# Kernel optimization log

Hardware: AMD Instinct MI355X
Metric: run time of the kernel (lower is better)

## Reference

```python
import jax, jax.numpy as jnp
import numpy as np

EMBED = 1024
HEADS = 16
HEAD_DIM = EMBED // HEADS
HIDDEN = 4096
EPS = 1e-5


def setup_inputs() -> dict:
    key = jax.random.key(0)
    ks = jax.random.split(key, 16)
    s_e = 1.0 / np.sqrt(EMBED)
    s_h = 1.0 / np.sqrt(HIDDEN)
    return {
        "x": jax.random.normal(ks[0], (8, 1024, EMBED), dtype=jnp.float32),
        "ln1_g": jnp.ones((EMBED,), jnp.float32),
        "ln1_b": jnp.zeros((EMBED,), jnp.float32),
        "ln2_g": jnp.ones((EMBED,), jnp.float32),
        "ln2_b": jnp.zeros((EMBED,), jnp.float32),
        "wq": jax.random.uniform(ks[1], (EMBED, EMBED), jnp.float32, -s_e, s_e),
        "bq": jax.random.uniform(ks[2], (EMBED,), jnp.float32, -s_e, s_e),
        "wk": jax.random.uniform(ks[3], (EMBED, EMBED), jnp.float32, -s_e, s_e),
        "bk": jax.random.uniform(ks[4], (EMBED,), jnp.float32, -s_e, s_e),
        "wv": jax.random.uniform(ks[5], (EMBED, EMBED), jnp.float32, -s_e, s_e),
        "bv": jax.random.uniform(ks[6], (EMBED,), jnp.float32, -s_e, s_e),
        "wo": jax.random.uniform(ks[7], (EMBED, EMBED), jnp.float32, -s_e, s_e),
        "bo": jax.random.uniform(ks[8], (EMBED,), jnp.float32, -s_e, s_e),
        "w1": jax.random.uniform(ks[9], (EMBED, HIDDEN), jnp.float32, -s_e, s_e),
        "b1": jax.random.uniform(ks[10], (HIDDEN,), jnp.float32, -s_e, s_e),
        "w2": jax.random.uniform(ks[11], (HIDDEN, EMBED), jnp.float32, -s_h, s_h),
        "b2": jax.random.uniform(ks[12], (EMBED,), jnp.float32, -s_h, s_h),
    }


def _layernorm(x, g, b):
    mu = jnp.mean(x, axis=-1, keepdims=True)
    var = jnp.mean((x - mu) ** 2, axis=-1, keepdims=True)
    return (x - mu) * jax.lax.rsqrt(var + EPS) * g + b


def reference(x, ln1_g, ln1_b, ln2_g, ln2_b, wq, bq, wk, bk, wv, bv, wo, bo, w1, b1, w2, b2):
    B, N, E = x.shape
    scale = HEAD_DIM ** (-0.5)
    # --- attention sublayer (pre-norm) ---
    h = _layernorm(x, ln1_g, ln1_b)
    q = (h @ wq + bq).reshape(B, N, HEADS, HEAD_DIM).transpose(0, 2, 1, 3) * scale
    k = (h @ wk + bk).reshape(B, N, HEADS, HEAD_DIM).transpose(0, 2, 1, 3)
    v = (h @ wv + bv).reshape(B, N, HEADS, HEAD_DIM).transpose(0, 2, 1, 3)
    scores = jnp.einsum("bhqd,bhkd->bhqk", q, k)
    attn = jax.nn.softmax(scores, axis=-1)
    ctx = jnp.einsum("bhqk,bhkd->bhqd", attn, v)
    ctx = ctx.transpose(0, 2, 1, 3).reshape(B, N, E)
    x = x + (ctx @ wo + bo)
    # --- FFN sublayer (pre-norm) ---
    h2 = _layernorm(x, ln2_g, ln2_b)
    ff = jax.nn.relu(h2 @ w1 + b1) @ w2 + b2
    return x + ff
```

## Files before the change

kernel.cpp:

```cpp
#include <hip/hip_runtime.h>
#include <hip/hip_bf16.h>

typedef __attribute__((ext_vector_type(4))) float f32x4;
typedef __attribute__((ext_vector_type(16))) float f32x16;
typedef __attribute__((ext_vector_type(8))) __bf16 bf16x8;
typedef __attribute__((ext_vector_type(4))) __bf16 bf16x4;
typedef __attribute__((ext_vector_type(4))) unsigned int u32x4;

static constexpr int E    = 1024;
static constexpr int TOK  = 8192;
static constexpr int HID  = 4096;

#define DEVINL __device__ __forceinline__

DEVINL void gload16(const void* g, void* l) {
  __builtin_amdgcn_global_load_lds((__attribute__((address_space(1))) void*)g,
                                   (__attribute__((address_space(3))) void*)l, 16, 0, 0);
}

#define ABAR()  asm volatile("s_barrier" ::: "memory")
#define AVM(n)  asm volatile("s_waitcnt vmcnt(" #n ")" ::: "memory")
#define ALGKM0() asm volatile("s_waitcnt lgkmcnt(0)")
#define CVTPK(dst, lo, hi) asm("v_cvt_pk_bf16_f32 %0, %1, %2" : "=v"(dst) : "v"(lo), "v"(hi))
#define PLSWAP(a, b) asm("v_permlane32_swap_b32 %0, %1" : "+v"(a), "+v"(b))

template <int N> DEVINL void avm() {
  if constexpr (N == 0)      asm volatile("s_waitcnt vmcnt(0)" ::: "memory");
  else if constexpr (N == 2) asm volatile("s_waitcnt vmcnt(2)" ::: "memory");
  else if constexpr (N == 6) asm volatile("s_waitcnt vmcnt(6)" ::: "memory");
  else if constexpr (N == 8) asm volatile("s_waitcnt vmcnt(8)" ::: "memory");
  else if constexpr (N == 9) asm volatile("s_waitcnt vmcnt(9)" ::: "memory");
  else                       asm volatile("s_waitcnt vmcnt(0)" ::: "memory");
}

__global__ __launch_bounds__(256) void wconv6_kernel(const float* __restrict__ wq,
                                                     const float* __restrict__ wk,
                                                     const float* __restrict__ wv,
                                                     const float* __restrict__ wo,
                                                     const float* __restrict__ w1,
                                                     const float* __restrict__ w2,
                                                     __bf16* __restrict__ Wqkv,
                                                     __bf16* __restrict__ Wot,
                                                     __bf16* __restrict__ W1t,
                                                     __bf16* __restrict__ W2t) {
  const int id = blockIdx.x;
  const float* W; __bf16* Wt; int K, N, lid;
  if (id < 1024)      { W = wq; Wt = Wqkv;                K = 1024; N = 1024; lid = id; }
  else if (id < 2048) { W = wk; Wt = Wqkv + 1024 * 1024;  K = 1024; N = 1024; lid = id - 1024; }
  else if (id < 3072) { W = wv; Wt = Wqkv + 2048 * 1024;  K = 1024; N = 1024; lid = id - 2048; }
  else if (id < 4096) { W = wo; Wt = Wot;                 K = 1024; N = 1024; lid = id - 3072; }
  else if (id < 8192) { W = w1; Wt = W1t;                 K = 1024; N = 4096; lid = id - 4096; }
  else                { W = w2; Wt = W2t;                 K = 4096; N = 1024; lid = id - 8192; }
  const int nx = N >> 5;
  const long n0 = (long)(lid % nx) * 32;
  const long k0 = (long)(lid / nx) * 32;

  __shared__ float tile[32][33];
  const int t  = threadIdx.x;
  const int r  = t >> 3;
  const int c4 = (t & 7) * 4;
  float4 v = *(const float4*)&W[(k0 + r) * N + n0 + c4];
  tile[r][c4 + 0] = v.x; tile[r][c4 + 1] = v.y;
  tile[r][c4 + 2] = v.z; tile[r][c4 + 3] = v.w;
  __syncthreads();
  bf16x4 o;
#pragma unroll
  for (int i = 0; i < 4; ++i) o[i] = (__bf16)tile[c4 + i][r];
  *(bf16x4*)&Wt[(n0 + r) * K + k0 + c4] = o;
}

__global__ __launch_bounds__(256) void ln_kernel(const float* __restrict__ X,
                                                 const float* __restrict__ g,
                                                 const float* __restrict__ be,
                                                 __bf16* __restrict__ O) {
  const int t = threadIdx.x;
  const long row = blockIdx.x;
  float4 v = *(const float4*)&X[row * E + t * 4];
  float s  = v.x + v.y + v.z + v.w;
  float ss = v.x * v.x + v.y * v.y + v.z * v.z + v.w * v.w;
#pragma unroll
  for (int off = 32; off; off >>= 1) {
    s  += __shfl_down(s, off);
    ss += __shfl_down(ss, off);
  }
  __shared__ float red[8];
  const int w = t >> 6;
  if ((t & 63) == 0) { red[w] = s; red[4 + w] = ss; }
  __syncthreads();
  s  = red[0] + red[1] + red[2] + red[3];
  ss = red[4] + red[5] + red[6] + red[7];
  const float mean = s * (1.0f / E);
  const float var  = ss * (1.0f / E) - mean * mean;
  const float rstd = rsqrtf(var + 1e-5f);
  float4 gv = *(const float4*)&g[t * 4];
  float4 bv = *(const float4*)&be[t * 4];
  bf16x4 o;
  o[0] = (__bf16)((v.x - mean) * rstd * gv.x + bv.x);
  o[1] = (__bf16)((v.y - mean) * rstd * gv.y + bv.y);
  o[2] = (__bf16)((v.z - mean) * rstd * gv.z + bv.z);
  o[3] = (__bf16)((v.w - mean) * rstd * gv.w + bv.w);
  *(bf16x4*)&O[row * E + t * 4] = o;
}

__global__ __launch_bounds__(256) void reduce2_kernel(float* __restrict__ out,
                                                      const __bf16* __restrict__ t0,
                                                      const __bf16* __restrict__ t1,
                                                      const float* __restrict__ b2) {
  const int i = blockIdx.x * 256 + threadIdx.x;
  float4 o = ((const float4*)out)[i];
  bf16x4 a = ((const bf16x4*)t0)[i];
  bf16x4 b = ((const bf16x4*)t1)[i];
  float4 bb = ((const float4*)b2)[i & 255];
  o.x += bb.x + (float)a[0] + (float)b[0];
  o.y += bb.y + (float)a[1] + (float)b[1];
  o.z += bb.z + (float)a[2] + (float)b[2];
  o.w += bb.w + (float)a[3] + (float)b[3];
  ((float4*)out)[i] = o;
}

template <bool RELU, bool RESID, bool OUTBF, int NB>
__global__ __launch_bounds__(512, 2) void gemm8p_kernel(const __bf16* __restrict__ A,
                                                        const __bf16* __restrict__ Bt,
                                                        const float* __restrict__ bias0,
                                                        const float* __restrict__ bias1,
                                                        const float* __restrict__ bias2,
                                                        const float* resid,
                                                        void* Cout, void* Cout2,
                                                        int M, int N, int K, int KLD) {
  extern __shared__ char lds[];
  const int tid  = threadIdx.x;
  const int lane = tid & 63;
  const int l15  = lane & 15;
  const int kp   = lane >> 4;
  const int wid  = tid >> 6;
  const int wr   = wid >> 2;
  const int wc   = wid & 3;

  const int gx   = gridDim.x, gy = gridDim.y;
  const int nwg  = gx * gy * gridDim.z;
  const int flat = blockIdx.x + gx * (blockIdx.y + gy * blockIdx.z);
  const int swz  = (flat & 7) * (nwg >> 3) + (flat >> 3);
  const int bx   = swz % gx;
  const int by   = (swz / gx) % gy;
  const int bz   = swz / (gx * gy);
  const long brow = (long)by * 256;
  const long bcol = (long)bx * 256;
  const long koff = (long)bz * K;

  const __bf16* Ab = A  + brow * KLD + koff;
  const __bf16* Bb = Bt + bcol * KLD + koff;
  void* Cdst = bz ? Cout2 : Cout;
  const int NT = K >> 6;

  auto stageU = [&](const __bf16* Gb, int rc0, int k0, int dstOff) {
#pragma unroll
    for (int i = 0; i < 2; ++i) {
      const int c = i * 512 + tid;
      const int r = c >> 3;
      const int p = (c & 7) ^ (r & 7);
      gload16(Gb + (long)(rc0 + r) * KLD + k0 + p * 8, lds + dstOff + c * 16);
    }
  };

  f32x4 acc[8][4];
  const f32x4 z4 = {0.f, 0.f, 0.f, 0.f};
#pragma unroll
  for (int m = 0; m < 8; ++m)
#pragma unroll
    for (int n = 0; n < 4; ++n) acc[m][n] = z4;

  bf16x8 af[4][2], bh0[2][2], bh1[2][2];

  auto readA = [&](int off) {
#pragma unroll
    for (int mm = 0; mm < 4; ++mm)
#pragma unroll
      for (int kk = 0; kk < 2; ++kk) {
        const int lr = mm * 32 + wr * 16 + l15;
        const int p  = ((kk << 2) + kp) ^ (lr & 7);
        af[mm][kk] = *(const bf16x8*)(lds + off + lr * 128 + p * 16);
      }
  };
  auto readB = [&](int off, bf16x8 (*bf)[2]) {
#pragma unroll
    for (int nn = 0; nn < 2; ++nn)
#pragma unroll
      for (int kk = 0; kk < 2; ++kk) {
        const int lc = nn * 64 + wc * 16 + l15;
        const int p  = ((kk << 2) + kp) ^ (lc & 7);
        bf[nn][kk] = *(const bf16x8*)(lds + off + lc * 128 + p * 16);
      }
  };
  auto quad = [&](int mb, int nb, bf16x8 (*bf)[2]) {
    __builtin_amdgcn_s_setprio(1);
#pragma unroll
    for (int kk = 0; kk < 2; ++kk)
#pragma unroll
      for (int mm = 0; mm < 4; ++mm)
#pragma unroll
        for (int nn = 0; nn < 2; ++nn)
          acc[mb + mm][nb + nn] = __builtin_amdgcn_mfma_f32_16x16x32_bf16(
              af[mm][kk], bf[nn][kk], acc[mb + mm][nb + nn], 0, 0, 0);
    __builtin_amdgcn_s_setprio(0);
  };

  stageU(Ab, 0,   0, 0);
  stageU(Bb, 0,   0, 32768);
  stageU(Bb, 128, 0, 49152);
  stageU(Ab, 128, 0, 16384);
  stageU(Ab, 0,   64, 65536 + 0);
  stageU(Bb, 0,   64, 65536 + 32768);
  stageU(Bb, 128, 64, 65536 + 49152);
  avm<6>();
  ABAR();

  for (int t = 0; t < NT; ++t) {
    const int cb  = (t & 1) ? 65536 : 0;
    const int nb1 = cb ^ 65536;
    const int k1 = (t + 1 < NT) ? ((t + 1) << 6) : 0;
    const int k2 = (t + 2 < NT) ? ((t + 2) << 6) : 0;

    readA(cb + 0);
    readB(cb + 32768, bh0);
    stageU(Ab, 128, k1, nb1 + 16384);
    ABAR(); ALGKM0();
    quad(0, 0, bh0);
    ABAR();

    readB(cb + 49152, bh1);
    stageU(Ab, 0, k2, cb + 0);
    ABAR(); ALGKM0();
    quad(0, 2, bh1);
    ABAR();

    readA(cb + 16384);
    stageU(Bb, 0, k2, cb + 32768);
    ABAR(); ALGKM0();
    quad(4, 0, bh0);
    ABAR();

    stageU(Bb, 128, k2, cb + 49152);
    avm<6>();
    ABAR();
    quad(4, 2, bh1);
    ABAR();
  }
  avm<0>();

#pragma unroll
  for (int m = 0; m < 8; ++m) {
#pragma unroll
    for (int n = 0; n < 4; ++n) {
      const long col = bcol + n * 64 + wc * 16 + l15;
      float bb;
      if (NB == 3) {
        const float* bp = (col < 1024) ? bias0 : ((col < 2048) ? bias1 : bias2);
        bb = bp[col & 1023];
      } else if (NB == 1) {
        bb = bias0[col];
      } else {
        bb = 0.f;
      }
#pragma unroll
      for (int j = 0; j < 4; ++j) {
        const long row = brow + m * 32 + wr * 16 + (lane >> 4) * 4 + j;
        float val = acc[m][n][j] + bb;
        if (RELU) val = fmaxf(val, 0.f);
        const long idx = row * N + col;
        if (RESID) val += resid[idx];
        if (OUTBF) ((__bf16*)Cdst)[idx] = (__bf16)val;
        else       ((float*)Cdst)[idx]  = val;
      }
    }
  }
}

template <int BM_, int DEPTH, bool RELU, bool RESID, bool OUTBF, int NB>
__global__ __launch_bounds__(512, 2) void gemmk_kernel(const __bf16* __restrict__ A,
                                                       const __bf16* __restrict__ Bt,
                                                       const float* __restrict__ bias0,
                                                       const float* __restrict__ bias1,
                                                       const float* __restrict__ bias2,
                                                       const float* resid,
                                                       void* Cout, void* Cout2,
                                                       int M, int N, int K, int KLD) {
  extern __shared__ char lds[];
  constexpr int MF    = BM_ / 32;
  constexpr int ABYT  = BM_ * 64;
  constexpr int TILEB = ABYT + 16384;
  constexpr int AL    = BM_ / 128;
  constexpr int TL    = AL + 2;
  constexpr int W     = (DEPTH - 2) * TL;

  const int tid  = threadIdx.x;
  const int lane = tid & 63;
  const int l15  = lane & 15;
  const int kp   = lane >> 4;
  const int wid  = tid >> 6;
  const int wr   = wid >> 2;
  const int wc   = wid & 3;

  const int gx   = gridDim.x, gy = gridDim.y;
  const int nwg  = gx * gy * gridDim.z;
  const int flat = blockIdx.x + gx * (blockIdx.y + gy * blockIdx.z);
  const int swz  = (flat & 7) * (nwg >> 3) + (flat >> 3);
  const int bx   = swz % gx;
  const int by   = (swz / gx) % gy;
  const int bz   = swz / (gx * gy);
  const long brow = (long)by * BM_;
  const long bcol = (long)bx * 256;
  const long koff = (long)bz * K;

  const __bf16* Ab = A  + brow * KLD + koff;
  const __bf16* Bb = Bt + bcol * KLD + koff;
  void* Cdst = bz ? Cout2 : Cout;
  const int NT = K >> 5;

  auto stageA = [&](int k0, char* dst) {
#pragma unroll
    for (int i = 0; i < AL; ++i) {
      const int c = i * 512 + tid;
      const int r = c >> 2;
      const int p = (c & 3) ^ ((r >> 1) & 3);
      gload16(Ab + (long)r * KLD + k0 + p * 8, dst + c * 16);
    }
  };
  auto stageB = [&](int k0, char* dst) {
#pragma unroll
    for (int i = 0; i < 2; ++i) {
      const int c = i * 512 + tid;
      const int r = c >> 2;
      const int p = (c & 3) ^ ((r >> 1) & 3);
      gload16(Bb + (long)r * KLD + k0 + p * 8, dst + c * 16);
    }
  };

  f32x4 acc[MF][4];
  const f32x4 z4 = {0.f, 0.f, 0.f, 0.f};
#pragma unroll
  for (int m = 0; m < MF; ++m)
#pragma unroll
    for (int n = 0; n < 4; ++n) acc[m][n] = z4;

#pragma unroll
  for (int pt = 0; pt < DEPTH - 1; ++pt) {
    stageA(pt * 32, lds + pt * TILEB);
    stageB(pt * 32, lds + pt * TILEB + ABYT);
  }

  bf16x8 af[4], bfr[4];

  for (int t = 0; t < NT; ++t) {
    const int cb = t % DEPTH;
    const int sb = (t + DEPTH - 1) % DEPTH;
    const char* Ac = lds + cb * TILEB;
    const char* Bc = Ac + ABYT;
    char* An = lds + sb * TILEB;
    const int kt = (t + DEPTH - 1 < NT) ? ((t + DEPTH - 1) << 5) : 0;

    avm<W>();
    ABAR();

#pragma unroll
    for (int m = 0; m < 4; ++m) {
      const int row = m * 32 + wr * 16 + l15;
      af[m] = *(const bf16x8*)(Ac + row * 64 + (kp ^ ((row >> 1) & 3)) * 16);
    }
#pragma unroll
    for (int n = 0; n < 4; ++n) {
      const int col = n * 64 + wc * 16 + l15;
      bfr[n] = *(const bf16x8*)(Bc + col * 64 + (kp ^ ((col >> 1) & 3)) * 16);
    }
    stageA(kt, An);
    stageB(kt, An + ABYT);
    ABAR(); ALGKM0();
    __builtin_amdgcn_s_setprio(1);
#pragma unroll
    for (int m = 0; m < 4; ++m)
#pragma unroll
      for (int n = 0; n < 4; ++n)
        acc[m][n] = __builtin_amdgcn_mfma_f32_16x16x32_bf16(af[m], bfr[n], acc[m][n], 0, 0, 0);
    __builtin_amdgcn_s_setprio(0);
  }
  avm<0>();

#pragma unroll
  for (int m = 0; m < MF; ++m) {
#pragma unroll
    for (int n = 0; n < 4; ++n) {
      const long col = bcol + n * 64 + wc * 16 + l15;
      float bb;
      if (NB == 3) {
        const float* bp = (col < 1024) ? bias0 : ((col < 2048) ? bias1 : bias2);
        bb = bp[col & 1023];
      } else if (NB == 1) {
        bb = bias0[col];
      } else {
        bb = 0.f;
      }
#pragma unroll
      for (int j = 0; j < 4; ++j) {
        const long row = brow + m * 32 + wr * 16 + (lane >> 4) * 4 + j;
        float val = acc[m][n][j] + bb;
        if (RELU) val = fmaxf(val, 0.f);
        const long idx = row * N + col;
        if (RESID) val += resid[idx];
        if (OUTBF) ((__bf16*)Cdst)[idx] = (__bf16)val;
        else       ((float*)Cdst)[idx]  = val;
      }
    }
  }
}

__global__ __launch_bounds__(256, 3) void attn_kernel(const __bf16* __restrict__ QKV,
                                                      __bf16* __restrict__ Og) {
  __shared__ __align__(16) __bf16 Qs[128 * 64];
  __shared__ __align__(16) __bf16 Ks[2][64 * 64];
  __shared__ __align__(16) __bf16 Vt[2][64 * 64];

  const int QSTR = 3072;
  const int t    = threadIdx.x;
  const int lane = t & 63;
  const int w    = t >> 6;
  const int l31  = lane & 31;
  const int h    = lane >> 5;
  const int b    = blockIdx.y >> 4;
  const int hh   = blockIdx.y & 15;
  const long row0 = (long)b * 1024 + (long)blockIdx.x * 128;
  const long kvrow0 = (long)b * 1024;
  const int colQ = hh * 64;
  const int colK = colQ + 1024;
  const int colV = colQ + 2048;

#pragma unroll
  for (int j = 0; j < 4; ++j) {
    const int c = j * 256 + t;
    const int r = c >> 3;
    const int p = (c & 7) ^ (r & 7);
    gload16(QKV + (row0 + r) * QSTR + colQ + p * 8, (char*)Qs + c * 16);
  }
#pragma unroll
  for (int j = 0; j < 2; ++j) {
    const int c = j * 256 + t;
    const int r = c >> 3;
    const int p = (c & 7) ^ (r & 7);
    gload16(QKV + (kvrow0 + r) * QSTR + colK + p * 8, (char*)Ks[0] + c * 16);
  }
  bf16x8 vv[2];
#pragma unroll
  for (int j = 0; j < 2; ++j) {
    const int c = j * 256 + t;
    const int key = c >> 3, dc = c & 7;
    vv[j] = *(const bf16x8*)(QKV + (kvrow0 + key) * QSTR + colV + dc * 8);
  }
  AVM(0);
#pragma unroll
  for (int j = 0; j < 2; ++j) {
    const int c = j * 256 + t;
    const int key = c >> 3, dc = c & 7;
#pragma unroll
    for (int e = 0; e < 8; ++e) {
      const int d = dc * 8 + e;
      *(__bf16*)((char*)Vt[0] + d * 128 + (((key >> 3) ^ dc) * 16) + (key & 7) * 2) = vv[j][e];
    }
  }
  __syncthreads();

  bf16x8 bq[4];
  {
    const int qrow = w * 32 + l31;
#pragma unroll
    for (int kk = 0; kk < 4; ++kk) {
      const int p = (kk * 2 + h) ^ (qrow & 7);
      bq[kk] = *(const bf16x8*)((const char*)Qs + qrow * 128 + p * 16);
    }
  }

  f32x16 ctx0, ctx1;
#pragma unroll
  for (int r = 0; r < 16; ++r) { ctx0[r] = 0.f; ctx1[r] = 0.f; }
  float m = -INFINITY, l = 0.f;

  for (int kb = 0; kb < 16; ++kb) {
    const int cur = kb & 1, nxt = cur ^ 1;
    const int kb1 = (kb + 1 < 16) ? kb + 1 : kb;
    const long kr1 = kvrow0 + kb1 * 64;

#pragma unroll
    for (int j = 0; j < 2; ++j) {
      const int c = j * 256 + t;
      const int key = c >> 3, dc = c & 7;
      vv[j] = *(const bf16x8*)(QKV + (kr1 + key) * QSTR + colV + dc * 8);
    }
#pragma unroll
    for (int j = 0; j < 2; ++j) {
      const int c = j * 256 + t;
      const int r = c >> 3;
      const int p = (c & 7) ^ (r & 7);
      gload16(QKV + (kr1 + r) * QSTR + colK + p * 8, (char*)Ks[nxt] + c * 16);
    }

    f32x16 s0, s1;
#pragma unroll
    for (int r = 0; r < 16; ++r) { s0[r] = 0.f; s1[r] = 0.f; }
    __builtin_amdgcn_s_setprio(1);
#pragma unroll
    for (int kk = 0; kk < 4; ++kk) {
      const int pce = kk * 2 + h;
      const int p0i = pce ^ (l31 & 7);
      bf16x8 ak0 = *(const bf16x8*)((const char*)Ks[cur] + l31 * 128 + p0i * 16);
      bf16x8 ak1 = *(const bf16x8*)((const char*)Ks[cur] + (32 + l31) * 128 + p0i * 16);
      s0 = __builtin_amdgcn_mfma_f32_32x32x16_bf16(ak0, bq[kk], s0, 0, 0, 0);
      s1 = __builtin_amdgcn_mfma_f32_32x32x16_bf16(ak1, bq[kk], s1, 0, 0, 0);
    }
    __builtin_amdgcn_s_setprio(0);

    float mx = s0[0];
#pragma unroll
    for (int r = 1; r < 16; ++r) mx = fmaxf(mx, s0[r]);
#pragma unroll
    for (int r = 0; r < 16; ++r) mx = fmaxf(mx, s1[r]);
    mx = fmaxf(mx, __shfl_xor(mx, 32));

    if (!__all(mx - m <= 64.f)) {
      const float mn = fmaxf(m, mx);
      const float corr = __expf((m - mn) * 0.125f);
      l *= corr;
#pragma unroll
      for (int r = 0; r < 16; ++r) { ctx0[r] *= corr; ctx1[r] *= corr; }
      m = mn;
    }
    f32x16 p0, p1;
    float rs = 0.f;
#pragma unroll
    for (int r = 0; r < 16; ++r) { p0[r] = __expf((s0[r] - m) * 0.125f); rs += p0[r]; }
#pragma unroll
    for (int r = 0; r < 16; ++r) { p1[r] = __expf((s1[r] - m) * 0.125f); rs += p1[r]; }
    rs += __shfl_xor(rs, 32);
    l += rs;

    AVM(2);
#pragma unroll
    for (int j = 0; j < 2; ++j) {
      const int c = j * 256 + t;
      const int key = c >> 3, dc = c & 7;
#pragma unroll
      for (int e = 0; e < 8; ++e) {
        const int d = dc * 8 + e;
        *(__bf16*)((char*)Vt[nxt] + d * 128 + (((key >> 3) ^ dc) * 16) + (key & 7) * 2) = vv[j][e];
      }
    }

    bf16x8 paf[4];
#pragma unroll
    for (int ks = 0; ks < 4; ++ks) {
      const int base = (ks & 1) * 8;
      unsigned a0, a1, b0, b1;
      if (ks < 2) {
        CVTPK(a0, p0[base + 0], p0[base + 1]);
        CVTPK(b0, p0[base + 4], p0[base + 5]);
        CVTPK(a1, p0[base + 2], p0[base + 3]);
        CVTPK(b1, p0[base + 6], p0[base + 7]);
      } else {
        CVTPK(a0, p1[base + 0], p1[base + 1]);
        CVTPK(b0, p1[base + 4], p1[base + 5]);
        CVTPK(a1, p1[base + 2], p1[base + 3]);
        CVTPK(b1, p1[base + 6], p1[base + 7]);
      }
      PLSWAP(a0, b0);
      PLSWAP(a1, b1);
      u32x4 wv4; wv4[0] = a0; wv4[1] = a1; wv4[2] = b0; wv4[3] = b1;
      paf[ks] = __builtin_bit_cast(bf16x8, wv4);
    }

    __builtin_amdgcn_s_setprio(1);
#pragma unroll
    for (int ks = 0; ks < 4; ++ks) {
      const int pce = ks * 2 + h;
      bf16x8 av0 = *(const bf16x8*)((const char*)Vt[cur] + l31 * 128 + ((pce ^ (l31 >> 3)) * 16));
      bf16x8 av1 = *(const bf16x8*)((const char*)Vt[cur] + (32 + l31) * 128 + ((pce ^ (4 + (l31 >> 3))) * 16));
      ctx0 = __builtin_amdgcn_mfma_f32_32x32x16_bf16(av0, paf[ks], ctx0, 0, 0, 0);
      ctx1 = __builtin_amdgcn_mfma_f32_32x32x16_bf16(av1, paf[ks], ctx1, 0, 0, 0);
    }
    __builtin_amdgcn_s_setprio(0);

    __syncthreads();
  }

  const float inv = 1.0f / l;
  const long orow = row0 + w * 32 + l31;
#pragma unroll
  for (int f = 0; f < 2; ++f)
#pragma unroll
    for (int tq = 0; tq < 4; ++tq) {
      bf16x4 o;
#pragma unroll
      for (int e = 0; e < 4; ++e) {
        const float v = (f ? ctx1[tq * 4 + e] : ctx0[tq * 4 + e]) * inv;
        o[e] = (__bf16)v;
      }
      const int col = colQ + f * 32 + tq * 8 + h * 4;
      *(bf16x4*)&Og[orow * E + col] = o;
    }
}

extern "C" void kernel_launch(void* const* d_in, const int* in_sizes, int n_in,
                              void* d_out, int out_size, void* d_ws, size_t ws_size,
                              hipStream_t stream) {
  const float* x     = (const float*)d_in[0];
  const float* ln1g  = (const float*)d_in[1];
  const float* ln1b  = (const float*)d_in[2];
  const float* ln2g  = (const float*)d_in[3];
  const float* ln2b  = (const float*)d_in[4];
  const float* wq    = (const float*)d_in[5];
  const float* bq    = (const float*)d_in[6];
  const float* wk    = (const float*)d_in[7];
  const float* bk    = (const float*)d_in[8];
  const float* wv    = (const float*)d_in[9];
  const float* bv    = (const float*)d_in[10];
  const float* wo    = (const float*)d_in[11];
  const float* bo    = (const float*)d_in[12];
  const float* w1    = (const float*)d_in[13];
  const float* b1    = (const float*)d_in[14];
  const float* w2    = (const float*)d_in[15];
  const float* b2    = (const float*)d_in[16];
  float* out = (float*)d_out;

  char* ws = (char*)d_ws;
  const size_t MB = 1024 * 1024;
  __bf16* Wqkv = (__bf16*)(ws + 0 * MB);
  __bf16* Wot  = (__bf16*)(ws + 6 * MB);
  __bf16* W1t  = (__bf16*)(ws + 8 * MB);
  __bf16* W2t  = (__bf16*)(ws + 16 * MB);
  __bf16* h    = (__bf16*)(ws + 24 * MB);
  __bf16* qkv  = (__bf16*)(ws + 40 * MB);
  __bf16* ctx  = (__bf16*)(ws + 88 * MB);
  __bf16* ff1  = (__bf16*)(ws + 40 * MB);
  __bf16* tmp0 = (__bf16*)(ws + 0 * MB);
  __bf16* tmp1 = (__bf16*)(ws + 24 * MB);

  const dim3 blk(256);
  const dim3 blk512(512);
  const size_t GLDS8P  = 131072;
  const size_t GLDS128 = 5 * (128 * 64 + 16384);

  wconv6_kernel<<<12288, blk, 0, stream>>>(wq, wk, wv, wo, w1, w2,
                                           Wqkv, Wot, W1t, W2t);

  ln_kernel<<<TOK, blk, 0, stream>>>(x, ln1g, ln1b, h);

  gemm8p_kernel<false, false, true, 3><<<dim3(3072 / 256, TOK / 256), blk512, GLDS8P, stream>>>(
      h, Wqkv, bq, bk, bv, nullptr, qkv, nullptr, TOK, 3072, E, E);

  attn_kernel<<<dim3(8, 128), blk, 0, stream>>>(qkv, ctx);

  gemmk_kernel<128, 5, false, true, false, 1><<<dim3(E / 256, TOK / 128), blk512, GLDS128, stream>>>(
      ctx, Wot, bo, nullptr, nullptr, x, out, nullptr, TOK, E, E, E);

  ln_kernel<<<TOK, blk, 0, stream>>>(out, ln2g, ln2b, h);

  gemm8p_kernel<true, false, true, 1><<<dim3(HID / 256, TOK / 256), blk512, GLDS8P, stream>>>(
      h, W1t, b1, nullptr, nullptr, nullptr, ff1, nullptr, TOK, HID, E, E);

  gemm8p_kernel<false, false, true, 0><<<dim3(E / 256, TOK / 256, 2), blk512, GLDS8P, stream>>>(
      ff1, W2t, nullptr, nullptr, nullptr, nullptr, tmp0, tmp1, TOK, E, HID / 2, HID);

  reduce2_kernel<<<TOK * E / 1024, blk, 0, stream>>>(out, tmp0, tmp1, b2);
}
```

Baseline: 347.9 us.

## Stage bf16 GEMM epilogue through LDS for coalesced stores; load Q directly

For bf16-output GEMMs, the epilogue now writes biased and activated results into a swizzled LDS tile, then writes them out as coalesced 16-byte vector stores. This replaces scattered 2-byte global stores. The attention kernel drops its Q shared-memory staging and loads each lane's Q fragment straight from global into registers, which frees LDS and may raise occupancy. The costs are an extra barrier plus an LDS round trip in the epilogue, and less coalesced Q loads.

```diff
diff --git a/kernel.cpp b/kernel.cpp
--- a/kernel.cpp
+++ b/kernel.cpp
@@ -246,30 +246,60 @@
     ABAR();
   }
   avm<0>();
-
-#pragma unroll
-  for (int m = 0; m < 8; ++m) {
-#pragma unroll
-    for (int n = 0; n < 4; ++n) {
-      const long col = bcol + n * 64 + wc * 16 + l15;
-      float bb;
-      if (NB == 3) {
-        const float* bp = (col < 1024) ? bias0 : ((col < 2048) ? bias1 : bias2);
-        bb = bp[col & 1023];
-      } else if (NB == 1) {
-        bb = bias0[col];
-      } else {
-        bb = 0.f;
-      }
-#pragma unroll
-      for (int j = 0; j < 4; ++j) {
-        const long row = brow + m * 32 + wr * 16 + (lane >> 4) * 4 + j;
-        float val = acc[m][n][j] + bb;
-        if (RELU) val = fmaxf(val, 0.f);
-        const long idx = row * N + col;
-        if (RESID) val += resid[idx];
-        if (OUTBF) ((__bf16*)Cdst)[idx] = (__bf16)val;
-        else       ((float*)Cdst)[idx]  = val;
+  ABAR();
+
+  if constexpr (OUTBF) {
+#pragma unroll
+    for (int m = 0; m < 8; ++m) {
+#pragma unroll
+      for (int n = 0; n < 4; ++n) {
+        const int lc = n * 64 + wc * 16 + l15;
+        const long col = bcol + lc;
+        float bb;
+        if (NB == 3) {
+          const float* bp = (col < 1024) ? bias0 : ((col < 2048) ? bias1 : bias2);
+          bb = bp[col & 1023];
+        } else if (NB == 1) {
+          bb = bias0[col];
+        } else {
+          bb = 0.f;
+        }
+#pragma unroll
+        for (int j = 0; j < 4; ++j) {
+          const int r = m * 32 + wr * 16 + (lane >> 4) * 4 + j;
+          float val = acc[m][n][j] + bb;
+          if (RELU) val = fmaxf(val, 0.f);
+          const int cB = lc * 2;
+          *(__bf16*)(lds + r * 512 + (cB ^ (((r >> 2) & 3) << 5))) = (__bf16)val;
+        }
+      }
+    }
+    __syncthreads();
+#pragma unroll
+    for (int i = 0; i < 16; ++i) {
+      const int chunk = i * 512 + tid;
+      const int r  = chunk >> 5;
+      const int pc = chunk & 31;
+      const int cB = pc * 16;
+      bf16x8 v = *(const bf16x8*)(lds + r * 512 + (cB ^ (((r >> 2) & 3) << 5)));
+      *(bf16x8*)((__bf16*)Cdst + (brow + r) * (long)N + bcol + pc * 8) = v;
+    }
+  } else {
+#pragma unroll
+    for (int m = 0; m < 8; ++m) {
+#pragma unroll
+      for (int n = 0; n < 4; ++n) {
+        const long col = bcol + n * 64 + wc * 16 + l15;
+        float bb = (NB == 1) ? bias0[col] : 0.f;
+#pragma unroll
+        for (int j = 0; j < 4; ++j) {
+          const long row = brow + m * 32 + wr * 16 + (lane >> 4) * 4 + j;
+          float val = acc[m][n][j] + bb;
+          if (RELU) val = fmaxf(val, 0.f);
+          const long idx = row * N + col;
+          if (RESID) val += resid[idx];
+          ((float*)Cdst)[idx] = val;
+        }
       }
     }
   }
@@ -414,7 +444,6 @@
 
 __global__ __launch_bounds__(256, 3) void attn_kernel(const __bf16* __restrict__ QKV,
                                                       __bf16* __restrict__ Og) {
-  __shared__ __align__(16) __bf16 Qs[128 * 64];
   __shared__ __align__(16) __bf16 Ks[2][64 * 64];
   __shared__ __align__(16) __bf16 Vt[2][64 * 64];
 
@@ -432,13 +461,14 @@
   const int colK = colQ + 1024;
   const int colV = colQ + 2048;
 
-#pragma unroll
-  for (int j = 0; j < 4; ++j) {
-    const int c = j * 256 + t;
-    const int r = c >> 3;
-    const int p = (c & 7) ^ (r & 7);
-    gload16(QKV + (row0 + r) * QSTR + colQ + p * 8, (char*)Qs + c * 16);
-  }
+  bf16x8 bq[4];
+  {
+    const long qrow = row0 + w * 32 + l31;
+#pragma unroll
+    for (int kk = 0; kk < 4; ++kk)
+      bq[kk] = *(const bf16x8*)(QKV + qrow * QSTR + colQ + kk * 16 + h * 8);
+  }
+
 #pragma unroll
   for (int j = 0; j < 2; ++j) {
     const int c = j * 256 + t;
@@ -465,16 +495,6 @@
     }
   }
   __syncthreads();
-
-  bf16x8 bq[4];
-  {
-    const int qrow = w * 32 + l31;
-#pragma unroll
-    for (int kk = 0; kk < 4; ++kk) {
-      const int p = (kk * 2 + h) ^ (qrow & 7);
-      bq[kk] = *(const bf16x8*)((const char*)Qs + qrow * 128 + p * 16);
-    }
-  }
 
   f32x16 ctx0, ctx1;
 #pragma unroll
```

Measured after the change: 353.2 us. No clear change (+1.5%).

## Enlarge attention block to 256 queries with 512 threads sharing K/V tiles

Applied to the files above, without the earlier changes.

The attention kernel now processes 256 query rows per block with 8 waves instead of 128 rows with 4 waves. Each staged K/V tile is shared by twice as many waves, which halves the global K/V traffic per query. Each thread now loads one chunk of K and V instead of two, and the wait count is adjusted to match. The grid shrinks to 512 blocks, which may reduce occupancy and load balance across CUs.

```diff
diff --git a/kernel.cpp b/kernel.cpp
--- a/kernel.cpp
+++ b/kernel.cpp
@@ -26,10 +26,9 @@
 
 template <int N> DEVINL void avm() {
   if constexpr (N == 0)      asm volatile("s_waitcnt vmcnt(0)" ::: "memory");
+  else if constexpr (N == 1) asm volatile("s_waitcnt vmcnt(1)" ::: "memory");
   else if constexpr (N == 2) asm volatile("s_waitcnt vmcnt(2)" ::: "memory");
   else if constexpr (N == 6) asm volatile("s_waitcnt vmcnt(6)" ::: "memory");
-  else if constexpr (N == 8) asm volatile("s_waitcnt vmcnt(8)" ::: "memory");
-  else if constexpr (N == 9) asm volatile("s_waitcnt vmcnt(9)" ::: "memory");
   else                       asm volatile("s_waitcnt vmcnt(0)" ::: "memory");
 }
 
@@ -412,9 +411,9 @@
   }
 }
 
-__global__ __launch_bounds__(256, 3) void attn_kernel(const __bf16* __restrict__ QKV,
+__global__ __launch_bounds__(512, 2) void attn_kernel(const __bf16* __restrict__ QKV,
                                                       __bf16* __restrict__ Og) {
-  __shared__ __align__(16) __bf16 Qs[128 * 64];
+  __shared__ __align__(16) __bf16 Qs[256 * 64];
   __shared__ __align__(16) __bf16 Ks[2][64 * 64];
   __shared__ __align__(16) __bf16 Vt[2][64 * 64];
 
@@ -426,7 +425,7 @@
   const int h    = lane >> 5;
   const int b    = blockIdx.y >> 4;
   const int hh   = blockIdx.y & 15;
-  const long row0 = (long)b * 1024 + (long)blockIdx.x * 128;
+  const long row0 = (long)b * 1024 + (long)blockIdx.x * 256;
   const long kvrow0 = (long)b * 1024;
   const int colQ = hh * 64;
   const int colK = colQ + 1024;
@@ -434,34 +433,29 @@
 
 #pragma unroll
   for (int j = 0; j < 4; ++j) {
-    const int c = j * 256 + t;
+    const int c = j * 512 + t;
     const int r = c >> 3;
     const int p = (c & 7) ^ (r & 7);
     gload16(QKV + (row0 + r) * QSTR + colQ + p * 8, (char*)Qs + c * 16);
   }
-#pragma unroll
-  for (int j = 0; j < 2; ++j) {
-    const int c = j * 256 + t;
+  {
+    const int c = t;
     const int r = c >> 3;
     const int p = (c & 7) ^ (r & 7);
     gload16(QKV + (kvrow0 + r) * QSTR + colK + p * 8, (char*)Ks[0] + c * 16);
   }
-  bf16x8 vv[2];
-#pragma unroll
-  for (int j = 0; j < 2; ++j) {
-    const int c = j * 256 + t;
-    const int key = c >> 3, dc = c & 7;
-    vv[j] = *(const bf16x8*)(QKV + (kvrow0 + key) * QSTR + colV + dc * 8);
+  bf16x8 vv;
+  {
+    const int key = t >> 3, dc = t & 7;
+    vv = *(const bf16x8*)(QKV + (kvrow0 + key) * QSTR + colV + dc * 8);
   }
   AVM(0);
-#pragma unroll
-  for (int j = 0; j < 2; ++j) {
-    const int c = j * 256 + t;
-    const int key = c >> 3, dc = c & 7;
+  {
+    const int key = t >> 3, dc = t & 7;
 #pragma unroll
     for (int e = 0; e < 8; ++e) {
       const int d = dc * 8 + e;
-      *(__bf16*)((char*)Vt[0] + d * 128 + (((key >> 3) ^ dc) * 16) + (key & 7) * 2) = vv[j][e];
+      *(__bf16*)((char*)Vt[0] + d * 128 + (((key >> 3) ^ dc) * 16) + (key & 7) * 2) = vv[e];
     }
   }
   __syncthreads();
@@ -486,15 +480,12 @@
     const int kb1 = (kb + 1 < 16) ? kb + 1 : kb;
     const long kr1 = kvrow0 + kb1 * 64;
 
-#pragma unroll
-    for (int j = 0; j < 2; ++j) {
-      const int c = j * 256 + t;
-      const int key = c >> 3, dc = c & 7;
-      vv[j] = *(const bf16x8*)(QKV + (kr1 + key) * QSTR + colV + dc * 8);
-    }
-#pragma unroll
-    for (int j = 0; j < 2; ++j) {
-      const int c = j * 256 + t;
+    {
+      const int key = t >> 3, dc = t & 7;
+      vv = *(const bf16x8*)(QKV + (kr1 + key) * QSTR + colV + dc * 8);
+    }
+    {
+      const int c = t;
       const int r = c >> 3;
       const int p = (c & 7) ^ (r & 7);
       gload16(QKV + (kr1 + r) * QSTR + colK + p * 8, (char*)Ks[nxt] + c * 16);
@@ -539,15 +530,13 @@
     rs += __shfl_xor(rs, 32);
     l += rs;
 
-    AVM(2);
-#pragma unroll
-    for (int j = 0; j < 2; ++j) {
-      const int c = j * 256 + t;
-      const int key = c >> 3, dc = c & 7;
+    AVM(1);
+    {
+      const int key = t >> 3, dc = t & 7;
 #pragma unroll
       for (int e = 0; e < 8; ++e) {
         const int d = dc * 8 + e;
-        *(__bf16*)((char*)Vt[nxt] + d * 128 + (((key >> 3) ^ dc) * 16) + (key & 7) * 2) = vv[j][e];
+        *(__bf16*)((char*)Vt[nxt] + d * 128 + (((key >> 3) ^ dc) * 16) + (key & 7) * 2) = vv[e];
       }
     }
 
@@ -652,7 +641,7 @@
   gemm8p_kernel<false, false, true, 3><<<dim3(3072 / 256, TOK / 256), blk512, GLDS8P, stream>>>(
       h, Wqkv, bq, bk, bv, nullptr, qkv, nullptr, TOK, 3072, E, E);
 
-  attn_kernel<<<dim3(8, 128), blk, 0, stream>>>(qkv, ctx);
+  attn_kernel<<<dim3(4, 128), blk512, 0, stream>>>(qkv, ctx);
 
   gemmk_kernel<128, 5, false, true, false, 1><<<dim3(E / 256, TOK / 128), blk512, GLDS128, stream>>>(
       ctx, Wot, bo, nullptr, nullptr, x, out, nullptr, TOK, E, E, E);
```

Result: slower. 357.1 us (+2.6%).
